# Optimization experiments

Measured on AMD Instinct MI355X. Metric: run time of the kernel, lower is better.

## Reference

```python
import jax, jax.numpy as jnp
import numpy as np

B, T, DIM, H = 2, 2048, 1024, 16
HD = DIM // H  # head_dim = 64
ROPE_BASE = 10000.0


def setup_inputs() -> dict:
    key = jax.random.key(0)
    k1, k2, k3, k4 = jax.random.split(key, 4)
    s = 1.0 / np.sqrt(DIM)
    return {
        "x": jax.random.normal(k1, (B, T, DIM), dtype=jnp.float32),
        "Wqkv": jax.random.normal(k2, (DIM, 3 * DIM), dtype=jnp.float32) * s,
        "Wout": jax.random.normal(k3, (DIM, DIM), dtype=jnp.float32) * s,
        "bout": jax.random.normal(k4, (DIM,), dtype=jnp.float32) * 0.01,
    }


def _rotate_half(x):
    # interleaved rotation: (x0,x1,x2,x3,...) -> (-x1,x0,-x3,x2,...)
    x1 = x[..., ::2]
    x2 = x[..., 1::2]
    return jnp.stack((-x2, x1), axis=-1).reshape(x.shape)


def _rope_cos_sin(seq_len, dtype):
    inv_freq = 1.0 / (ROPE_BASE ** (jnp.arange(0, HD, 2, dtype=jnp.float32) / HD))
    t = jnp.arange(seq_len, dtype=jnp.float32)
    freqs = t[:, None] * inv_freq[None, :]          # [T, HD/2]
    emb = jnp.concatenate((freqs, freqs), axis=-1)  # [T, HD] (cat layout, as in source)
    return jnp.cos(emb).astype(dtype), jnp.sin(emb).astype(dtype)


def reference(x, Wqkv, Wout, bout):
    b, t, _ = x.shape
    qkv = x @ Wqkv                                  # [B, T, 3*DIM]
    q, k, v = jnp.split(qkv, 3, axis=-1)
    # b t (h d) -> b h t d
    reshape = lambda z: z.reshape(b, t, H, HD).transpose(0, 2, 1, 3)
    q, k, v = reshape(q), reshape(k), reshape(v)
    cos, sin = _rope_cos_sin(t, x.dtype)            # [T, HD]
    q = q * cos + _rotate_half(q) * sin
    k = k * cos + _rotate_half(k) * sin
    scale = HD ** -0.5
    scores = jnp.einsum("bhqd,bhkd->bhqk", q, k) * scale
    attn = jax.nn.softmax(scores, axis=-1)
    out = jnp.einsum("bhqk,bhkd->bhqd", attn, v)    # [B, H, T, HD]
    out = out.transpose(0, 2, 1, 3).reshape(b, t, DIM)
    return out @ Wout + bout
```

## Files before the change

### kernel.cpp

```cpp
#include <hip/hip_runtime.h>
#include <math.h>


typedef unsigned short u16;
typedef __attribute__((ext_vector_type(8))) short short8;
typedef __attribute__((ext_vector_type(4))) short short4v;
typedef __attribute__((ext_vector_type(4))) float f32x4;
typedef __attribute__((ext_vector_type(16))) float f32x16;

#define T_SEQ 2048

#if __has_builtin(__builtin_amdgcn_exp2f)
#define EXP2(x) __builtin_amdgcn_exp2f(x)
#else
#define EXP2(x) exp2f(x)
#endif

__device__ __forceinline__ float b2f(u16 u) {
    union { unsigned int i; float f; } x; x.i = ((unsigned int)u) << 16; return x.f;
}
__device__ __forceinline__ u16 f2b(float f) {
    union { float f; unsigned int i; } x; x.f = f;
    return (u16)((x.i + 0x7FFFu + ((x.i >> 16) & 1u)) >> 16);
}
__device__ __forceinline__ void gl_lds16(const u16* g, u16* l) {
    __builtin_amdgcn_global_load_lds(
        (const __attribute__((address_space(1))) unsigned int*)g,
        (__attribute__((address_space(3))) unsigned int*)l, 16, 0, 0);
}
__device__ __forceinline__ unsigned int packpair(float a, float b) {
    union { float f; unsigned int u; } xa, xb; xa.f = a; xb.f = b;
    return (xa.u >> 16) | (xb.u & 0xffff0000u);
}

__global__ __launch_bounds__(256) void setup_kernel(
    const float* __restrict__ x, const float* __restrict__ Wqkv,
    const float* __restrict__ Wout, u16* __restrict__ xb,
    u16* __restrict__ WqkvT, u16* __restrict__ WoutT,
    float* __restrict__ costab, float* __restrict__ sintab)
{
    const int bid = blockIdx.x;
    const int tid = threadIdx.x;

    if (bid < 4096) {
        int i = (bid * 256 + tid) * 4;
        float4 v = *(const float4*)(x + i);
        ushort4 w;
        w.x = f2b(v.x); w.y = f2b(v.y); w.z = f2b(v.z); w.w = f2b(v.w);
        *(ushort4*)(xb + i) = w;
        return;
    }
    if (bid < 8192) {
        const float* in; u16* out; int R, Cn, bx, by;
        if (bid < 7168) { in = Wqkv; out = WqkvT; R = 1024; Cn = 3072;
                          int id = bid - 4096; bx = id % 96; by = id / 96; }
        else            { in = Wout; out = WoutT; R = 1024; Cn = 1024;
                          int id = bid - 7168; bx = id & 31; by = id >> 5; }
        __shared__ u16 tile[32][33];
        const int tx = tid & 31, ty = tid >> 5;
        const int r0 = by * 32, c0 = bx * 32;
#pragma unroll
        for (int rr = ty; rr < 32; rr += 8)
            tile[tx][rr] = f2b(in[(size_t)(r0 + rr) * Cn + c0 + tx]);
        __syncthreads();
#pragma unroll
        for (int rr = ty; rr < 32; rr += 8)
            out[(size_t)(c0 + rr) * R + r0 + tx] = tile[rr][tx];
        return;
    }
    {
        int idx = (bid - 8192) * 256 + tid;
        int t = idx >> 6, d = idx & 63;
        const float nl32 = -0.28782313662425576f;
        float f = __expf((float)(d & 31) * nl32);
        float s, c;
        __sincosf((float)t * f, &s, &c);
        costab[idx] = c; sintab[idx] = s;
    }
}

template<int OBF>
__global__ __launch_bounds__(256) void gemm_bt_mfma(
    const u16* __restrict__ A, const u16* __restrict__ Bt,
    void* __restrict__ Cv, const float* __restrict__ bias,
    int M, int N, int K)
{
    __shared__ u16 As[128 * 32];
    __shared__ u16 Bs[128 * 32];

    const int tid = threadIdx.x;
    const int wave = tid >> 6, lane = tid & 63;
    const int col = lane & 15, quad = lane >> 4;
    const int wm = (wave & 1) * 64, wn = (wave >> 1) * 64;
    const int m0 = blockIdx.y * 128, n0 = blockIdx.x * 128;

    f32x4 acc[4][4];
#pragma unroll
    for (int i = 0; i < 4; ++i)
#pragma unroll
        for (int j = 0; j < 4; ++j) acc[i][j] = f32x4{0.f, 0.f, 0.f, 0.f};

    const int c1 = tid, c2 = tid + 256;
    const u16* a1 = A + (size_t)(m0 + (c1 >> 2)) * K + (c1 & 3) * 8;
    const u16* a2 = A + (size_t)(m0 + (c2 >> 2)) * K + (c2 & 3) * 8;
    const u16* b1 = Bt + (size_t)(n0 + (c1 >> 2)) * K + (c1 & 3) * 8;
    const u16* b2 = Bt + (size_t)(n0 + (c2 >> 2)) * K + (c2 & 3) * 8;
    u16* la1 = As + c1 * 8; u16* la2 = As + c2 * 8;
    u16* lb1 = Bs + c1 * 8; u16* lb2 = Bs + c2 * 8;

    for (int k0 = 0; k0 < K; k0 += 32) {
        __syncthreads();
        gl_lds16(a1 + k0, la1);
        gl_lds16(a2 + k0, la2);
        gl_lds16(b1 + k0, lb1);
        gl_lds16(b2 + k0, lb2);
        __syncthreads();

        short8 af[4], bfr[4];
#pragma unroll
        for (int i = 0; i < 4; ++i) {
            af[i]  = *(const short8*)&As[(wm + i * 16 + col) * 32 + quad * 8];
            bfr[i] = *(const short8*)&Bs[(wn + i * 16 + col) * 32 + quad * 8];
        }
#pragma unroll
        for (int i = 0; i < 4; ++i)
#pragma unroll
            for (int j = 0; j < 4; ++j)
                acc[i][j] = __builtin_amdgcn_mfma_f32_16x16x32_bf16(
                    af[i], bfr[j], acc[i][j], 0, 0, 0);
    }

#pragma unroll
    for (int j = 0; j < 4; ++j) {
        int n = n0 + wn + j * 16 + col;
        float bv = bias ? bias[n] : 0.f;
#pragma unroll
        for (int i = 0; i < 4; ++i) {
            int mbase = m0 + wm + i * 16 + quad * 4;
#pragma unroll
            for (int r = 0; r < 4; ++r) {
                if (OBF) ((u16*)Cv)[(size_t)(mbase + r) * N + n] = f2b(acc[i][j][r] + bv);
                else     ((float*)Cv)[(size_t)(mbase + r) * N + n] = acc[i][j][r] + bv;
            }
        }
    }
}

__global__ __launch_bounds__(256) void prep_kernel(
    const u16* __restrict__ qkvb, const float* __restrict__ costab,
    const float* __restrict__ sintab, u16* __restrict__ Qb,
    u16* __restrict__ Kb, u16* __restrict__ Vimg)
{
    __shared__ u16 Vls[64][72];

    const int tid = threadIdx.x;
    const int bh = blockIdx.y;
    const int t0 = blockIdx.x * 64;
    const int b = bh >> 4, h = bh & 15;
    const int t_loc = tid >> 2;
    const int d0 = (tid & 3) * 16;

    const int t = t0 + t_loc;
    const u16* qp = qkvb + ((size_t)(b * T_SEQ + t)) * 3072 + h * 64 + d0;

    float ct[16], st[16];
    {
        const float* cp = costab + (size_t)t * 64 + d0;
        const float* sp = sintab + (size_t)t * 64 + d0;
#pragma unroll
        for (int j = 0; j < 16; j += 4) {
            *(float4*)&ct[j] = *(const float4*)(cp + j);
            *(float4*)&st[j] = *(const float4*)(sp + j);
        }
    }

#pragma unroll
    for (int part = 0; part < 2; ++part) {
        const float sc = part ? 1.f : 0.18033688011112042f;
        const u16* src = qp + part * 1024;
        u16* dst = (part ? Kb : Qb) + ((size_t)(bh * T_SEQ + t)) * 64 + d0;
        short8 v0 = *(const short8*)(src);
        short8 v1 = *(const short8*)(src + 8);
        float f[16];
#pragma unroll
        for (int j = 0; j < 8; ++j) { f[j] = b2f((u16)v0[j]); f[8 + j] = b2f((u16)v1[j]); }
        u16 o[16];
#pragma unroll
        for (int i = 0; i < 8; ++i) {
            float e = f[2 * i], od = f[2 * i + 1];
            o[2 * i]     = f2b((e * ct[2 * i]      - od * st[2 * i]) * sc);
            o[2 * i + 1] = f2b((od * ct[2 * i + 1] + e  * st[2 * i + 1]) * sc);
        }
        *(short8*)(dst)     = *(short8*)&o[0];
        *(short8*)(dst + 8) = *(short8*)&o[8];
    }

    {
        const u16* src = qp + 2048;
        *(short8*)&Vls[t_loc][d0]     = *(const short8*)(src);
        *(short8*)&Vls[t_loc][d0 + 8] = *(const short8*)(src + 8);
    }
    __syncthreads();
    {
        const int m_  = (tid >> 7) & 1;
        const int db  = (tid >> 6) & 1;
        const int h2  = (tid >> 5) & 1;
        const int dv  = tid & 31;
        const int k0v = m_ * 16 + h2 * 8;
        const int dcol = db * 32 + dv;
        const int kt_base = blockIdx.x * 2;
#pragma unroll
        for (int ktl = 0; ktl < 2; ++ktl) {
            u16 o[8];
#pragma unroll
            for (int j = 0; j < 8; ++j)
                o[j] = Vls[ktl * 32 + k0v + j][dcol];
            u16* dst = Vimg + ((size_t)(bh * 64 + kt_base + ktl)) * 2048 + tid * 8;
            *(short8*)dst = *(short8*)&o[0];
        }
    }
}

__global__ __launch_bounds__(256, 2) void attn32_kernel(
    const u16* __restrict__ Qb, const u16* __restrict__ Kb,
    const u16* __restrict__ Vimg, u16* __restrict__ aob)
{
    __shared__ u16 Kbuf[3][2048];
    __shared__ u16 Vbuf[3][2048];

    const int tid = threadIdx.x;
    const int wave = tid >> 6, lane = tid & 63;
    const int qcol = lane & 31;
    const int hi = lane >> 5;

    const int bid = blockIdx.x;
    const int lbid = (bid & 7) * 64 + (bid >> 3);
    const int bh = lbid >> 4;
    const int qblk = lbid & 15;
    const int qrow0 = qblk * 128 + wave * 32;

    short8 qa[4];
    {
        const u16* qp = Qb + ((size_t)(bh * T_SEQ + qrow0 + qcol)) * 64 + hi * 8;
#pragma unroll
        for (int c = 0; c < 4; ++c) qa[c] = *(const short8*)(qp + c * 16);
    }

    f32x16 O0, O1;
#pragma unroll
    for (int i = 0; i < 16; ++i) { O0[i] = 0.f; O1[i] = 0.f; }
    float Lacc = 0.f;

    const u16* kg_ptr = Kb + ((size_t)bh * T_SEQ + qcol) * 64 + wave * 16 + hi * 8;
    const u16* vg_ptr = Vimg + ((size_t)bh * 64) * 2048 + tid * 8;

#define STAGE(p, rr) do {                                                     \
        gl_lds16(kg_ptr + (size_t)(rr) * 2048, &Kbuf[p][tid * 8]);            \
        gl_lds16(vg_ptr + (size_t)(rr) * 2048, &Vbuf[p][tid * 8]);            \
    } while (0)

    STAGE(0, 0);
    STAGE(1, 1);

    int cur = 0, prv = 2;
    for (int r = 0; r < 64; ++r) {
        if (r < 63) asm volatile("s_waitcnt vmcnt(2)" ::: "memory");
        else        asm volatile("s_waitcnt vmcnt(0)" ::: "memory");
        __builtin_amdgcn_s_barrier();
        asm volatile("" ::: "memory");
        __builtin_amdgcn_sched_barrier(0);

        short8 kf[4], vA[4];
#pragma unroll
        for (int f = 0; f < 4; ++f)
            kf[f] = *(const short8*)&Kbuf[cur][(f * 64 + lane) * 8];
#pragma unroll
        for (int rg = 0; rg < 4; ++rg)
            vA[rg] = *(const short8*)&Vbuf[cur][rg * 512 + lane * 8];

        if (r < 62) STAGE(prv, r + 2);

        f32x16 sT;
#pragma unroll
        for (int ii = 0; ii < 16; ++ii) sT[ii] = 0.f;
        __builtin_amdgcn_s_setprio(1);
#pragma unroll
        for (int c = 0; c < 4; ++c)
            sT = __builtin_amdgcn_mfma_f32_32x32x16_bf16(kf[c], qa[c], sT, 0, 0, 0);
        __builtin_amdgcn_s_setprio(0);

        float pe[16];
#pragma unroll
        for (int ii = 0; ii < 16; ++ii) pe[ii] = EXP2(sT[ii]);
#pragma unroll
        for (int g = 0; g < 4; ++g)
            Lacc += (pe[4 * g + 0] + pe[4 * g + 1]) +
                    (pe[4 * g + 2] + pe[4 * g + 3]);

        unsigned int W0 = packpair(pe[0],  pe[1]);
        unsigned int W1 = packpair(pe[2],  pe[3]);
        unsigned int W2 = packpair(pe[4],  pe[5]);
        unsigned int W3 = packpair(pe[6],  pe[7]);
        unsigned int W4 = packpair(pe[8],  pe[9]);
        unsigned int W5 = packpair(pe[10], pe[11]);
        unsigned int W6 = packpair(pe[12], pe[13]);
        unsigned int W7 = packpair(pe[14], pe[15]);

        asm volatile("v_permlane32_swap_b32 %0, %1" : "+v"(W0), "+v"(W2));
        asm volatile("v_permlane32_swap_b32 %0, %1" : "+v"(W1), "+v"(W3));
        asm volatile("v_permlane32_swap_b32 %0, %1" : "+v"(W4), "+v"(W6));
        asm volatile("v_permlane32_swap_b32 %0, %1" : "+v"(W5), "+v"(W7));

        union FU { unsigned int u[4]; short8 s; } f0, f1;
        f0.u[0] = W0; f0.u[1] = W1; f0.u[2] = W2; f0.u[3] = W3;
        f1.u[0] = W4; f1.u[1] = W5; f1.u[2] = W6; f1.u[3] = W7;

        __builtin_amdgcn_s_setprio(1);
        O0 = __builtin_amdgcn_mfma_f32_32x32x16_bf16(vA[0], f0.s, O0, 0, 0, 0);
        O1 = __builtin_amdgcn_mfma_f32_32x32x16_bf16(vA[1], f0.s, O1, 0, 0, 0);
        O0 = __builtin_amdgcn_mfma_f32_32x32x16_bf16(vA[2], f1.s, O0, 0, 0, 0);
        O1 = __builtin_amdgcn_mfma_f32_32x32x16_bf16(vA[3], f1.s, O1, 0, 0, 0);
        __builtin_amdgcn_s_setprio(0);

        prv = cur;
        cur = (cur == 2) ? 0 : cur + 1;
    }
#undef STAGE

    float Lq = Lacc + __shfl(Lacc, lane ^ 32);
    float inv = 1.f / Lq;

    const int b = bh >> 4, h = bh & 15;
    u16* ab = aob + ((size_t)(b * T_SEQ + qrow0 + qcol)) * 1024 + h * 64;
#pragma unroll
    for (int g2 = 0; g2 < 4; ++g2) {
        int dd = g2 * 8 + hi * 4;
        ushort4 w0, w1;
        w0.x = f2b(O0[4 * g2 + 0] * inv); w0.y = f2b(O0[4 * g2 + 1] * inv);
        w0.z = f2b(O0[4 * g2 + 2] * inv); w0.w = f2b(O0[4 * g2 + 3] * inv);
        w1.x = f2b(O1[4 * g2 + 0] * inv); w1.y = f2b(O1[4 * g2 + 1] * inv);
        w1.z = f2b(O1[4 * g2 + 2] * inv); w1.w = f2b(O1[4 * g2 + 3] * inv);
        *(ushort4*)(ab + dd)      = w0;
        *(ushort4*)(ab + 32 + dd) = w1;
    }
}

extern "C" void kernel_launch(void* const* d_in, const int* in_sizes, int n_in,
                              void* d_out, int out_size, void* d_ws, size_t ws_size,
                              hipStream_t stream)
{
    const float* x    = (const float*)d_in[0];
    const float* Wqkv = (const float*)d_in[1];
    const float* Wout = (const float*)d_in[2];
    const float* bout = (const float*)d_in[3];
    float* out = (float*)d_out;

    char* w = (char*)d_ws;
    u16* qkvb    = (u16*)(w);
    u16* xb      = (u16*)(w + 25165824);
    u16* WqkvT   = (u16*)(w + 33554432);
    u16* WoutT   = (u16*)(w + 39845888);
    u16* aob     = (u16*)(w + 41943040);
    u16* Qb      = (u16*)(w + 50331648);
    u16* Kb      = (u16*)(w + 58720256);
    u16* Vimg    = (u16*)(w + 67108864);
    float* ctab  = (float*)(w + 75497472);
    float* stab  = (float*)(w + 76021760);

    dim3 blk(256);
    setup_kernel<<<dim3(8704), blk, 0, stream>>>(x, Wqkv, Wout, xb, WqkvT, WoutT, ctab, stab);
    gemm_bt_mfma<1><<<dim3(24, 32), blk, 0, stream>>>(xb, WqkvT, qkvb, nullptr, 4096, 3072, 1024);
    prep_kernel<<<dim3(32, 32), blk, 0, stream>>>(qkvb, ctab, stab, Qb, Kb, Vimg);
    attn32_kernel<<<dim3(512), blk, 0, stream>>>(Qb, Kb, Vimg, aob);
    gemm_bt_mfma<0><<<dim3(8, 32), blk, 0, stream>>>(aob, WoutT, out, bout, 4096, 1024, 1024);
}
```

Before: 199.2 us.

## Triple-buffer GEMM LDS loads with a single barrier, stage bf16 output through LDS

Replaces the single-buffered, two-barrier K loop in the MFMA GEMM with a three-stage LDS ring. Loads for step k+2 are issued while step k computes, with vmcnt waits and one barrier per iteration. MFMA priority is raised via s_setprio. The bf16 output path now stages the tile in padded LDS and writes coalesced 16-byte rows instead of scattered 2-byte stores. This raises LDS use to 48KB per block, which may lower occupancy, and it relies on the hand-written vmcnt counts being correct.

After: 189.9 us. 1.05x faster.

```diff
diff --git a/kernel.cpp b/kernel.cpp
--- a/kernel.cpp
+++ b/kernel.cpp
@@ -85,8 +85,9 @@
     void* __restrict__ Cv, const float* __restrict__ bias,
     int M, int N, int K)
 {
-    __shared__ u16 As[128 * 32];
-    __shared__ u16 Bs[128 * 32];
+    __shared__ u16 sbuf[24576];
+    u16* const As0 = sbuf;
+    u16* const Bs0 = sbuf + 12288;
 
     const int tid = threadIdx.x;
     const int wave = tid >> 6, lane = tid & 63;
@@ -105,42 +106,85 @@
     const u16* a2 = A + (size_t)(m0 + (c2 >> 2)) * K + (c2 & 3) * 8;
     const u16* b1 = Bt + (size_t)(n0 + (c1 >> 2)) * K + (c1 & 3) * 8;
     const u16* b2 = Bt + (size_t)(n0 + (c2 >> 2)) * K + (c2 & 3) * 8;
-    u16* la1 = As + c1 * 8; u16* la2 = As + c2 * 8;
-    u16* lb1 = Bs + c1 * 8; u16* lb2 = Bs + c2 * 8;
-
-    for (int k0 = 0; k0 < K; k0 += 32) {
-        __syncthreads();
-        gl_lds16(a1 + k0, la1);
-        gl_lds16(a2 + k0, la2);
-        gl_lds16(b1 + k0, lb1);
-        gl_lds16(b2 + k0, lb2);
-        __syncthreads();
+    const int l1 = c1 * 8, l2 = c2 * 8;
+
+#define GST(p, ks) do { const int k0_ = (ks) * 32;                            \
+        gl_lds16(a1 + k0_, As0 + (p) * 4096 + l1);                            \
+        gl_lds16(a2 + k0_, As0 + (p) * 4096 + l2);                            \
+        gl_lds16(b1 + k0_, Bs0 + (p) * 4096 + l1);                            \
+        gl_lds16(b2 + k0_, Bs0 + (p) * 4096 + l2);                            \
+    } while (0)
+
+    const int NK = K >> 5;
+    GST(0, 0);
+    GST(1, 1);
+
+    int cur = 0, prv = 2;
+    for (int ks = 0; ks < NK; ++ks) {
+        if (ks < NK - 1) asm volatile("s_waitcnt vmcnt(4)" ::: "memory");
+        else             asm volatile("s_waitcnt vmcnt(0)" ::: "memory");
+        __builtin_amdgcn_s_barrier();
+        asm volatile("" ::: "memory");
+        __builtin_amdgcn_sched_barrier(0);
 
         short8 af[4], bfr[4];
+        const u16* Ap = As0 + cur * 4096;
+        const u16* Bp = Bs0 + cur * 4096;
 #pragma unroll
         for (int i = 0; i < 4; ++i) {
-            af[i]  = *(const short8*)&As[(wm + i * 16 + col) * 32 + quad * 8];
-            bfr[i] = *(const short8*)&Bs[(wn + i * 16 + col) * 32 + quad * 8];
-        }
+            af[i]  = *(const short8*)&Ap[(wm + i * 16 + col) * 32 + quad * 8];
+            bfr[i] = *(const short8*)&Bp[(wn + i * 16 + col) * 32 + quad * 8];
+        }
+
+        if (ks < NK - 2) GST(prv, ks + 2);
+
+        __builtin_amdgcn_s_setprio(1);
 #pragma unroll
         for (int i = 0; i < 4; ++i)
 #pragma unroll
             for (int j = 0; j < 4; ++j)
                 acc[i][j] = __builtin_amdgcn_mfma_f32_16x16x32_bf16(
                     af[i], bfr[j], acc[i][j], 0, 0, 0);
-    }
-
-#pragma unroll
-    for (int j = 0; j < 4; ++j) {
-        int n = n0 + wn + j * 16 + col;
-        float bv = bias ? bias[n] : 0.f;
-#pragma unroll
-        for (int i = 0; i < 4; ++i) {
-            int mbase = m0 + wm + i * 16 + quad * 4;
-#pragma unroll
-            for (int r = 0; r < 4; ++r) {
-                if (OBF) ((u16*)Cv)[(size_t)(mbase + r) * N + n] = f2b(acc[i][j][r] + bv);
-                else     ((float*)Cv)[(size_t)(mbase + r) * N + n] = acc[i][j][r] + bv;
+        __builtin_amdgcn_s_setprio(0);
+
+        prv = cur;
+        cur = (cur == 2) ? 0 : cur + 1;
+    }
+#undef GST
+
+    if (OBF) {
+        __syncthreads();
+        u16* Cs = sbuf;
+#pragma unroll
+        for (int j = 0; j < 4; ++j) {
+            const int cl = wn + j * 16 + col;
+            const float bv = bias ? bias[n0 + cl] : 0.f;
+#pragma unroll
+            for (int i = 0; i < 4; ++i) {
+                const int rl = wm + i * 16 + quad * 4;
+#pragma unroll
+                for (int r = 0; r < 4; ++r)
+                    Cs[(rl + r) * 136 + cl] = f2b(acc[i][j][r] + bv);
+            }
+        }
+        __syncthreads();
+        const int row = tid >> 1, half = tid & 1;
+        const u16* src = Cs + row * 136 + half * 64;
+        u16* dst = (u16*)Cv + (size_t)(m0 + row) * N + n0 + half * 64;
+#pragma unroll
+        for (int s = 0; s < 8; ++s)
+            *(short8*)(dst + s * 8) = *(const short8*)(src + s * 8);
+    } else {
+#pragma unroll
+        for (int j = 0; j < 4; ++j) {
+            int n = n0 + wn + j * 16 + col;
+            float bv = bias ? bias[n] : 0.f;
+#pragma unroll
+            for (int i = 0; i < 4; ++i) {
+                int mbase = m0 + wm + i * 16 + quad * 4;
+#pragma unroll
+                for (int r = 0; r < 4; ++r)
+                    ((float*)Cv)[(size_t)(mbase + r) * N + n] = acc[i][j][r] + bv;
             }
         }
     }
```
